# Performance work log

Measured on AMD Instinct MI355X. Metric: run time of the kernel, lower is better.

## Reference

```python
import jax, jax.numpy as jnp
import numpy as np

# Config (matches init_kwargs)
N_HEAD, D_K, D_MODEL, D_INNER, N_LAYERS = 8, 64, 512, 2048, 4
VOCAB, PAD_IDX, REP_IDX, N_POSITION = 512, 0, 1, 200
B, N_NEAR, S = 64, 32, 12  # B batches, 32 near-POIs each, <=12 type tokens per POI
NPOI = B * N_NEAR


def sinusoid_table(n_position, d):
    pos = np.arange(n_position)[:, None].astype(np.float64)
    i = np.arange(d)[None, :]
    angle = pos / np.power(10000.0, 2 * (i // 2) / d)
    tab = np.zeros((n_position, d))
    tab[:, 0::2] = np.sin(angle[:, 0::2])
    tab[:, 1::2] = np.cos(angle[:, 1::2])
    return jnp.asarray(tab, jnp.float32)


def layer_norm(x, g, b, eps=1e-6):
    m = jnp.mean(x, -1, keepdims=True)
    v = jnp.var(x, -1, keepdims=True)
    return g * (x - m) * jax.lax.rsqrt(v + eps) + b


def pack_indices(npl, ttn):
    """Replace the torch Python-loop ragged pack with a single precomputed gather.
    Returns per-output-slot (poi_idx, tok_idx) and a validity mask [B, L]."""
    npl = np.asarray(npl); ttn = np.asarray(ttn)
    Bn = len(npl)
    ends = np.cumsum(npl); starts = ends - npl
    seq_len = np.array([1 + int(ttn[starts[b]:ends[b]].sum()) for b in range(Bn)])
    L = int(seq_len.max())  # == max_batch_len in the torch code
    poi_idx = np.zeros((Bn, L), np.int32)
    tok_idx = np.zeros((Bn, L), np.int32)
    for b in range(Bn):
        pos = 1  # slot 0 is the [REP] token
        for p in range(int(starts[b]), int(ends[b])):
            t = int(ttn[p])
            poi_idx[b, pos:pos + t] = p
            tok_idx[b, pos:pos + t] = np.arange(t)
            pos += t
    valid = np.arange(L)[None, :] < seq_len[:, None]  # pad_from_num_list(pad_num)
    return poi_idx, tok_idx, valid


def setup_inputs() -> dict:
    key = jax.random.key(0)
    ks = jax.random.split(key, 24)
    nrm = lambda k, shape, s=0.02: jax.random.normal(k, shape, jnp.float32) * s
    poi_type = jax.random.randint(ks[0], (NPOI, S), 0, VOCAB, jnp.int32)
    loc_emb = jax.random.normal(ks[1], (NPOI, D_MODEL), jnp.float32)
    near_pois_num_list = jnp.full((B,), N_NEAR, jnp.int32)
    type_token_num = jax.random.randint(ks[2], (NPOI,), 1, S + 1, jnp.int32)
    emb = nrm(ks[3], (VOCAB, D_MODEL), 1.0).at[PAD_IDX].set(0.0)  # padding_idx row zeroed
    return {
        "poi_type": poi_type, "loc_emb": loc_emb,
        "near_pois_num_list": near_pois_num_list, "type_token_num": type_token_num,
        "emb": emb,
        "Wq": nrm(ks[4], (N_LAYERS, D_MODEL, D_MODEL)),
        "Wk": nrm(ks[5], (N_LAYERS, D_MODEL, D_MODEL)),
        "Wv": nrm(ks[6], (N_LAYERS, D_MODEL, D_MODEL)),
        "Wo": nrm(ks[7], (N_LAYERS, D_MODEL, D_MODEL)),
        "bo": jnp.zeros((N_LAYERS, D_MODEL), jnp.float32),
        "ln1_g": jnp.ones((N_LAYERS, D_MODEL), jnp.float32),
        "ln1_b": jnp.zeros((N_LAYERS, D_MODEL), jnp.float32),
        "W1": nrm(ks[8], (N_LAYERS, D_MODEL, D_INNER)),
        "b1": jnp.zeros((N_LAYERS, D_INNER), jnp.float32),
        "W2": nrm(ks[9], (N_LAYERS, D_INNER, D_MODEL)),
        "b2": jnp.zeros((N_LAYERS, D_MODEL), jnp.float32),
        "ln2_g": jnp.ones((N_LAYERS, D_MODEL), jnp.float32),
        "ln2_b": jnp.zeros((N_LAYERS, D_MODEL), jnp.float32),
        "lnf_g": jnp.ones((D_MODEL,), jnp.float32),
        "lnf_b": jnp.zeros((D_MODEL,), jnp.float32),
    }


def encoder_forward(poi_type, loc_emb, poi_idx, tok_idx, tok_mask, attn_mask,
                    emb, Wq, Wk, Wv, Wo, bo, ln1_g, ln1_b, W1, b1, W2, b2,
                    ln2_g, ln2_b, lnf_g, lnf_b):
    pos_table = sinusoid_table(N_POSITION, D_MODEL)
    # embedding + positional encoding (dropout = eval/identity) + location broadcast
    enc = emb[poi_type] + pos_table[None, :S, :] + loc_emb[:, None, :]  # [NPOI, S, D]
    # fused ragged gather+pad (replaces the per-row torch.cat loop)
    x = jnp.where(tok_mask[..., None], enc[poi_idx, tok_idx], 0.0)      # [B, L, D]
    x = x.at[:, 0, :].set(emb[REP_IDX])                                  # [REP] token at slot 0
    x = layer_norm(x, lnf_g, lnf_b)
    Bn, L, D = x.shape
    inv_temp = np.float32(1.0 / np.sqrt(D_K))
    for l in range(N_LAYERS):
        # multi-head self-attention, post-LN residual
        q = (x @ Wq[l]).reshape(Bn, L, N_HEAD, D_K)
        k = (x @ Wk[l]).reshape(Bn, L, N_HEAD, D_K)
        v = (x @ Wv[l]).reshape(Bn, L, N_HEAD, D_K)
        scores = jnp.einsum('bqhd,bkhd->bhqk', q, k) * inv_temp
        scores = jnp.where(attn_mask[:, None, None, :], scores, -1e9)
        attn = jax.nn.softmax(scores, axis=-1)
        o = jnp.einsum('bhqk,bkhd->bqhd', attn, v).reshape(Bn, L, D)
        x = layer_norm(x + o @ Wo[l] + bo[l], ln1_g[l], ln1_b[l])
        # position-wise FFN, post-LN residual
        h = jax.nn.relu(x @ W1[l] + b1[l])
        x = layer_norm(x + h @ W2[l] + b2[l], ln2_g[l], ln2_b[l])
    return x


def reference(poi_type, loc_emb, near_pois_num_list, type_token_num,
              emb, Wq, Wk, Wv, Wo, bo, ln1_g, ln1_b, W1, b1, W2, b2,
              ln2_g, ln2_b, lnf_g, lnf_b):
    poi_idx, tok_idx, valid = pack_indices(np.asarray(near_pois_num_list),
                                           np.asarray(type_token_num))
    L = valid.shape[1]
    tok_mask = jnp.asarray(valid & (np.arange(L)[None, :] > 0))
    attn_mask = jnp.asarray(valid)
    out = encoder_forward(poi_type, loc_emb, jnp.asarray(poi_idx), jnp.asarray(tok_idx),
                          tok_mask, attn_mask, emb, Wq, Wk, Wv, Wo, bo,
                          ln1_g, ln1_b, W1, b1, W2, b2, ln2_g, ln2_b, lnf_g, lnf_b)
    return out, attn_mask
```

## Files before the change

### kernel.cpp

```cpp
#include <hip/hip_runtime.h>
#include <stdint.h>

#define DM 512
#define NH 8
#define DKH 64
#define DI 2048
#define NLAY 4
#define SMAX 12
#define BATCH 64
#define NPOI 2048
#define REPIDX 1
#define VOCAB 512

#define PLS 40
#define PLS2 264

#define S_POI 0
#define S_LOC 1
#define S_NPL 2
#define S_TTN 3
#define S_EMB 4
#define S_WQ 5
#define S_WK 6
#define S_WV 7
#define S_WO 8
#define S_BO 9
#define S_LN1G 10
#define S_LN1B 11
#define S_W1 12
#define S_B1 13
#define S_W2 14
#define S_B2 15
#define S_LN2G 16
#define S_LN2B 17
#define S_LNFG 18
#define S_LNFB 19

#define F_FD 0
#define F_SI 1

typedef unsigned short u16;
typedef short short8 __attribute__((ext_vector_type(8)));
typedef float f32x4 __attribute__((ext_vector_type(4)));
typedef const uint32_t __attribute__((address_space(1)))* as1_u32p;
typedef uint32_t __attribute__((address_space(3)))* as3_u32p;

__device__ __forceinline__ float bf2f(u16 u) {
    union { uint32_t i; float f; } v; v.i = (uint32_t)u << 16; return v.f;
}
__device__ __forceinline__ u16 f2bf(float f) {
    union { uint32_t i; float f; } v; v.f = f;
    uint32_t u = v.i;
    u += 0x7fffu + ((u >> 16) & 1u);
    return (u16)(u >> 16);
}
__device__ __forceinline__ float loadIn(const void* p, size_t i, int fd) {
    if (fd == 1) return bf2f(((const u16*)p)[i]);
    if (fd == 3) { union { u16 u; _Float16 h; } v; v.u = ((const u16*)p)[i]; return (float)v.h; }
    if (fd == 2) return (float)((const double*)p)[i];
    return ((const float*)p)[i];
}
__device__ __forceinline__ int loadInt(const void* p, size_t i, int istride) {
    return (int)((const uint32_t*)p)[i * istride];
}

__device__ __forceinline__ int xcd_swizzle(int lin, int nwg) {
    int qq = nwg >> 3, rr = nwg & 7;
    int xcd = lin & 7, off = lin >> 3;
    return (xcd < rr ? xcd * (qq + 1) : rr * (qq + 1) + (xcd - rr) * qq) + off;
}

__global__ void bind_kernel(void* a0, void* a1, void* a2, void* a3, void* a4,
                            void* c0, void* c1, void* c2, void* c3, void* c4, void* c5, void* c6,
                            void* f0, void* f1,
                            void* w40, void* w41,
                            void* poi, void* npl, void* emb, void* b1,
                            void** tab, int* flags) {
    if (threadIdx.x != 0 || blockIdx.x != 0) return;

    int fd = -1, gAt = -1;
    {
        const u16* a16 = (const u16*)f0; const uint32_t* a32 = (const uint32_t*)f0;
        const unsigned long long* a64 = (const unsigned long long*)f0;
        if (a16[0] == 0x3C00 && a16[1] == 0x3C00) { fd = 3; gAt = 0; }
        else if (a16[0] == 0x3F80 && a16[1] == 0x3F80) { fd = 1; gAt = 0; }
        else if (a32[0] == 0x3F800000u) { fd = 0; gAt = 0; }
        else if (a64[0] == 0x3FF0000000000000ull) { fd = 2; gAt = 0; }
        else {
            const u16* b16 = (const u16*)f1; const uint32_t* b32 = (const uint32_t*)f1;
            const unsigned long long* b64 = (const unsigned long long*)f1;
            if (b16[0] == 0x3C00 && b16[1] == 0x3C00) { fd = 3; gAt = 1; }
            else if (b16[0] == 0x3F80 && b16[1] == 0x3F80) { fd = 1; gAt = 1; }
            else if (b32[0] == 0x3F800000u) { fd = 0; gAt = 1; }
            else if (b64[0] == 0x3FF0000000000000ull) { fd = 2; gAt = 1; }
        }
        if (fd < 0) { fd = 0; gAt = 0; }
    }

    int sI = 1;
    {
        const uint32_t* n32 = (const uint32_t*)npl;
        if (n32[0] == 32u && n32[1] == 0u && n32[2] == 32u) sI = 2;
    }

    void* g1[5] = {a0, a1, a2, a3, a4};
    int locIdx = -1;
    for (int j = 0; j < 5 && locIdx < 0; ++j) {
        float mx = 0.f;
        for (int s = 0; s < 64; ++s) {
            float v = loadIn(g1[j], (size_t)s * 997 + 13, fd);
            mx = fmaxf(mx, fabsf(v));
        }
        if (mx > 0.5f) locIdx = j;
    }
    if (locIdx < 0) locIdx = 0;
    tab[S_LOC] = g1[locIdx];
    {
        int wslot[4] = {S_WQ, S_WK, S_WV, S_WO}; int wi = 0;
        for (int j = 0; j < 5; ++j) if (j != locIdx) tab[wslot[wi++]] = g1[j];
    }

    void* g2[7] = {c0, c1, c2, c3, c4, c5, c6};
    int ttnIdx = -1;
    for (int j = 0; j < 7 && ttnIdx < 0; ++j) {
        const uint32_t* u = (const uint32_t*)g2[j];
        bool ok = true;
        for (int s = 0; s < 24; ++s) {
            uint32_t lo = u[(size_t)s * sI];
            if (lo < 1u || lo > 12u) { ok = false; break; }
            if (sI == 2 && u[(size_t)s * 2 + 1] != 0u) { ok = false; break; }
        }
        if (ok) ttnIdx = j;
    }
    if (ttnIdx < 0) ttnIdx = 0;
    tab[S_TTN] = g2[ttnIdx];
    {
        int gslots[2] = {S_LN1G, S_LN2G}; int bslots[4] = {S_BO, S_LN1B, S_B2, S_LN2B};
        int gi = 0, bi = 0;
        for (int j = 0; j < 7; ++j) {
            if (j == ttnIdx) continue;
            float v0 = loadIn(g2[j], 0, fd);
            if (v0 > 0.5f && gi < 2) tab[gslots[gi++]] = g2[j];
            else if (bi < 4) tab[bslots[bi++]] = g2[j];
            else if (gi < 2) tab[gslots[gi++]] = g2[j];
        }
    }

    tab[S_LNFG] = gAt == 0 ? f0 : f1;
    tab[S_LNFB] = gAt == 0 ? f1 : f0;
    tab[S_W1] = w40; tab[S_W2] = w41;
    tab[S_POI] = poi; tab[S_NPL] = npl; tab[S_EMB] = emb; tab[S_B1] = b1;

    flags[F_FD] = fd;
    flags[F_SI] = sI;
}

__global__ void bind_positional(void* p0, void* p1, void* p2, void* p3, void* p4,
                                void* p5, void* p6, void* p7, void* p8, void* p9,
                                void* p10, void* p11, void* p12, void* p13, void* p14,
                                void* p15, void* p16, void* p17, void* p18, void* p19,
                                void** tab, int* flags) {
    if (threadIdx.x != 0) return;
    void* ps[20] = {p0,p1,p2,p3,p4,p5,p6,p7,p8,p9,p10,p11,p12,p13,p14,p15,p16,p17,p18,p19};
    for (int i = 0; i < 20; ++i) tab[i] = ps[i];
    flags[F_FD] = 0; flags[F_SI] = 1;
}

__global__ void sinusoid_kernel(float* __restrict__ tab) {
    int i = blockIdx.x * 256 + threadIdx.x;
    if (i >= SMAX * DM) return;
    int s = i / DM, d = i - s * DM;
    double expo = (double)(2 * (d / 2)) / (double)DM;
    double angle = (double)s / pow(10000.0, expo);
    tab[i] = (float)((d & 1) ? cos(angle) : sin(angle));
}

__global__ void pack_kernel(void* const* tab, const int* flags,
                            int* __restrict__ seq_len, int* __restrict__ poi_idx,
                            int* __restrict__ tok_idx, int L) {
    const void* npl = tab[S_NPL];
    const void* ttn = tab[S_TTN];
    const int sI = flags[F_SI];
    int b = threadIdx.x;
    if (b >= BATCH) return;
    int start = 0;
    for (int i = 0; i < b; ++i) start += loadInt(npl, i, sI);
    int cnt = loadInt(npl, b, sI);
    for (int j = 0; j < L; ++j) { poi_idx[b * L + j] = 0; tok_idx[b * L + j] = 0; }
    int pos = 1;
    for (int p = start; p < start + cnt; ++p) {
        int tn = loadInt(ttn, p, sI);
        for (int j = 0; j < tn; ++j) {
            if (pos < L) { poi_idx[b * L + pos] = p; tok_idx[b * L + pos] = j; ++pos; }
        }
    }
    seq_len[b] = pos;
}

__global__ __launch_bounds__(256) void build_enc(void* const* tab, const int* flags,
                                                 const float* __restrict__ pos_tab,
                                                 float* __restrict__ enc) {
    const int fd = flags[F_FD], sI = flags[F_SI];
    const void* poi_type = tab[S_POI];
    const void* loc_emb = tab[S_LOC];
    const void* emb = tab[S_EMB];
    int ps = blockIdx.x;
    int p = ps / SMAX, s = ps - p * SMAX;
    int tok = loadInt(poi_type, ps, sI);
    tok = tok < 0 ? 0 : (tok >= VOCAB ? VOCAB - 1 : tok);
    #pragma unroll
    for (int j = 0; j < 2; ++j) {
        int d = threadIdx.x + 256 * j;
        enc[(size_t)ps * DM + d] = loadIn(emb, (size_t)tok * DM + d, fd)
                                 + pos_tab[s * DM + d]
                                 + loadIn(loc_emb, (size_t)p * DM + d, fd);
    }
}

__global__ __launch_bounds__(256) void gather_ln_wave(void* const* tab, const int* flags,
                                                      const float* __restrict__ enc,
                                                      const int* __restrict__ poi_idx,
                                                      const int* __restrict__ tok_idx,
                                                      const int* __restrict__ seq_len,
                                                      float* __restrict__ x, u16* __restrict__ xb,
                                                      int L, int M) {
    const int fd = flags[F_FD];
    const void* emb = tab[S_EMB];
    const void* g = tab[S_LNFG];
    const void* bb = tab[S_LNFB];
    const int row = blockIdx.x * 4 + (threadIdx.x >> 6);
    if (row >= M) return;
    const int b = row / L, l = row - b * L;
    const int lane = threadIdx.x & 63;
    const int slen = seq_len[b];
    float e[8];
    if (l == 0) {
        #pragma unroll
        for (int j = 0; j < 8; ++j) e[j] = loadIn(emb, REPIDX * DM + lane + 64 * j, fd);
    } else if (l < slen) {
        int p = poi_idx[row];
        p = p < 0 ? 0 : (p >= NPOI ? NPOI - 1 : p);
        int t = tok_idx[row];
        t = t < 0 ? 0 : (t >= SMAX ? SMAX - 1 : t);
        const float* src = enc + ((size_t)p * SMAX + t) * DM;
        #pragma unroll
        for (int j = 0; j < 8; ++j) e[j] = src[lane + 64 * j];
    } else {
        #pragma unroll
        for (int j = 0; j < 8; ++j) e[j] = 0.f;
    }
    float s1 = 0.f, s2 = 0.f;
    #pragma unroll
    for (int j = 0; j < 8; ++j) { s1 += e[j]; s2 += e[j] * e[j]; }
    #pragma unroll
    for (int off = 1; off < 64; off <<= 1) {
        s1 += __shfl_xor(s1, off, 64);
        s2 += __shfl_xor(s2, off, 64);
    }
    float mean = s1 * (1.f / DM);
    float var = s2 * (1.f / DM) - mean * mean;
    float rs = rsqrtf(fmaxf(var, 0.f) + 1e-6f);
    #pragma unroll
    for (int j = 0; j < 8; ++j) {
        int d = lane + 64 * j;
        float o = loadIn(g, d, fd) * (e[j] - mean) * rs + loadIn(bb, d, fd);
        x[(size_t)row * DM + d] = o;
        xb[(size_t)row * DM + d] = f2bf(o);
    }
}

__global__ __launch_bounds__(256) void ln_wave(void* const* tab, const int* flags,
                                               float* __restrict__ x, const u16* __restrict__ t,
                                               int gslot, int bslot, int poff,
                                               u16* __restrict__ xb, int M) {
    const int fd = flags[F_FD];
    const void* g = tab[gslot];
    const void* bb = tab[bslot];
    const int row = blockIdx.x * 4 + (threadIdx.x >> 6);
    if (row >= M) return;
    const int lane = threadIdx.x & 63;
    float e[8];
    #pragma unroll
    for (int j = 0; j < 8; ++j) {
        int d = lane + 64 * j;
        e[j] = x[(size_t)row * DM + d] + bf2f(t[(size_t)row * DM + d]);
    }
    float s1 = 0.f, s2 = 0.f;
    #pragma unroll
    for (int j = 0; j < 8; ++j) { s1 += e[j]; s2 += e[j] * e[j]; }
    #pragma unroll
    for (int off = 1; off < 64; off <<= 1) {
        s1 += __shfl_xor(s1, off, 64);
        s2 += __shfl_xor(s2, off, 64);
    }
    float mean = s1 * (1.f / DM);
    float var = s2 * (1.f / DM) - mean * mean;
    float rs = rsqrtf(fmaxf(var, 0.f) + 1e-6f);
    #pragma unroll
    for (int j = 0; j < 8; ++j) {
        int d = lane + 64 * j;
        float o = loadIn(g, poff + d, fd) * (e[j] - mean) * rs + loadIn(bb, poff + d, fd);
        x[(size_t)row * DM + d] = o;
        xb[(size_t)row * DM + d] = f2bf(o);
    }
}

__global__ __launch_bounds__(256) void transpose_tiled(void* const* tab, const int* flags,
                                                       int srcslot, u16* __restrict__ dst,
                                                       int K, int N,
                                                       size_t srcStride, size_t dstStride) {
    __shared__ float ts[32][33];
    const int fd = flags[F_FD];
    const void* src = tab[srcslot];
    const int layer = blockIdx.y;
    const size_t soff = (size_t)layer * srcStride;
    u16* d = dst + (size_t)layer * dstStride;
    const int ntx = N >> 5;
    const int kt = blockIdx.x / ntx, nt = blockIdx.x - kt * ntx;
    const int tx = threadIdx.x & 31, ty = threadIdx.x >> 5;
    #pragma unroll
    for (int j = 0; j < 4; ++j)
        ts[ty + j * 8][tx] = loadIn(src, soff + (size_t)(kt * 32 + ty + j * 8) * N + nt * 32 + tx, fd);
    __syncthreads();
    #pragma unroll
    for (int j = 0; j < 4; ++j)
        d[(size_t)(nt * 32 + ty + j * 8) * K + kt * 32 + tx] = f2bf(ts[tx][ty + j * 8]);
}

__global__ void zero_u16(u16* __restrict__ p, int n) {
    int i = blockIdx.x * 256 + threadIdx.x;
    if (i < n) p[i] = 0;
}
__global__ void zero_vt(u16* __restrict__ vt, int L, int Lr) {
    int tail = Lr - L;
    int n = BATCH * DM * tail;
    int i = blockIdx.x * 256 + threadIdx.x;
    if (i < n) {
        int rd = i / tail;
        int kk = L + (i - rd * tail);
        vt[(size_t)rd * Lr + kk] = 0;
    }
}

template <bool RELU>
__global__ __launch_bounds__(512) void gemm_mfma(const u16* __restrict__ A, const u16* __restrict__ Bt,
                                                 void* const* tab, const int* flags,
                                                 int biasslot, int boff,
                                                 u16* __restrict__ C, int N, int K) {
    __shared__ __align__(16) u16 As[128 * 64];
    __shared__ __align__(16) u16 Bs[128 * 64];
    const int tid = threadIdx.x;
    const int lane = tid & 63;
    const int w = tid >> 6;
    const int wr = w & 3, wc = w >> 2;
    const int gy = gridDim.y;
    int lin = xcd_swizzle(blockIdx.x + gridDim.x * blockIdx.y, gridDim.x * gy);
    const int m0 = (lin / gy) * 128, n0 = (lin % gy) * 128;

    const int sr = tid >> 3;
    const int scb = (((lane & 7) ^ ((lane >> 3) & 7)) * 8);
    const int row_in = lane & 15;
    const int hi4 = lane >> 4;

    f32x4 acc[2][4];
    const f32x4 fz = {0.f, 0.f, 0.f, 0.f};
    #pragma unroll
    for (int i = 0; i < 2; ++i)
        #pragma unroll
        for (int j = 0; j < 4; ++j) acc[i][j] = fz;

    for (int k0 = 0; k0 < K; k0 += 64) {
        __syncthreads();
        #pragma unroll
        for (int j = 0; j < 2; ++j) {
            __builtin_amdgcn_global_load_lds(
                (as1_u32p)(const void*)(A + (size_t)(m0 + j * 64 + sr) * K + k0 + scb),
                (as3_u32p)(void*)(As + j * 4096 + w * 512), 16, 0, 0);
            __builtin_amdgcn_global_load_lds(
                (as1_u32p)(const void*)(Bt + (size_t)(n0 + j * 64 + sr) * K + k0 + scb),
                (as3_u32p)(void*)(Bs + j * 4096 + w * 512), 16, 0, 0);
        }
        __syncthreads();

        #pragma unroll
        for (int kk = 0; kk < 2; ++kk) {
            const int cb = ((kk * 4 + hi4) ^ (row_in & 7)) * 8;
            short8 af[2], bfr[4];
            #pragma unroll
            for (int mf = 0; mf < 2; ++mf)
                af[mf] = *(const short8*)&As[(wr * 32 + mf * 16 + row_in) * 64 + cb];
            #pragma unroll
            for (int nf = 0; nf < 4; ++nf)
                bfr[nf] = *(const short8*)&Bs[(wc * 64 + nf * 16 + row_in) * 64 + cb];
            #pragma unroll
            for (int mf = 0; mf < 2; ++mf)
                #pragma unroll
                for (int nf = 0; nf < 4; ++nf)
                    acc[mf][nf] = __builtin_amdgcn_mfma_f32_16x16x32_bf16(af[mf], bfr[nf], acc[mf][nf], 0, 0, 0);
        }
    }

    const int fd = flags[F_FD];
    #pragma unroll
    for (int nf = 0; nf < 4; ++nf) {
        int col = n0 + wc * 64 + nf * 16 + (lane & 15);
        float bv = (biasslot >= 0) ? loadIn(tab[biasslot], boff + col, fd) : 0.f;
        #pragma unroll
        for (int mf = 0; mf < 2; ++mf) {
            int rbase = m0 + wr * 32 + mf * 16 + (lane >> 4) * 4;
            #pragma unroll
            for (int r = 0; r < 4; ++r) {
                float v = acc[mf][nf][r] + bv;
                if (RELU) v = v > 0.f ? v : 0.f;
                C[(size_t)(rbase + r) * N + col] = f2bf(v);
            }
        }
    }
}

__global__ __launch_bounds__(512) void gemm_qkv(const u16* __restrict__ A, const u16* __restrict__ Bt,
                                                u16* __restrict__ qk, u16* __restrict__ vt,
                                                int L, int Lr, int M, int Mp) {
    __shared__ __align__(16) u16 As[128 * 64];
    __shared__ __align__(16) u16 Bs[128 * 64];
    const int tid = threadIdx.x;
    const int lane = tid & 63;
    const int w = tid >> 6;
    const int wr = w & 3, wc = w >> 2;
    const int gy = gridDim.y;
    int lin = xcd_swizzle(blockIdx.x + gridDim.x * blockIdx.y, gridDim.x * gy);
    const int m0 = (lin / gy) * 128, n0 = (lin % gy) * 128;

    const int sr = tid >> 3;
    const int scb = (((lane & 7) ^ ((lane >> 3) & 7)) * 8);
    const int row_in = lane & 15;
    const int hi4 = lane >> 4;

    f32x4 acc[2][4];
    const f32x4 fz = {0.f, 0.f, 0.f, 0.f};
    #pragma unroll
    for (int i = 0; i < 2; ++i)
        #pragma unroll
        for (int j = 0; j < 4; ++j) acc[i][j] = fz;

    for (int k0 = 0; k0 < DM; k0 += 64) {
        __syncthreads();
        #pragma unroll
        for (int j = 0; j < 2; ++j) {
            __builtin_amdgcn_global_load_lds(
                (as1_u32p)(const void*)(A + (size_t)(m0 + j * 64 + sr) * DM + k0 + scb),
                (as3_u32p)(void*)(As + j * 4096 + w * 512), 16, 0, 0);
            __builtin_amdgcn_global_load_lds(
                (as1_u32p)(const void*)(Bt + (size_t)(n0 + j * 64 + sr) * DM + k0 + scb),
                (as3_u32p)(void*)(Bs + j * 4096 + w * 512), 16, 0, 0);
        }
        __syncthreads();

        #pragma unroll
        for (int kk = 0; kk < 2; ++kk) {
            const int cb = ((kk * 4 + hi4) ^ (row_in & 7)) * 8;
            short8 af[2], bfr[4];
            #pragma unroll
            for (int mf = 0; mf < 2; ++mf)
                af[mf] = *(const short8*)&As[(wr * 32 + mf * 16 + row_in) * 64 + cb];
            #pragma unroll
            for (int nf = 0; nf < 4; ++nf)
                bfr[nf] = *(const short8*)&Bs[(wc * 64 + nf * 16 + row_in) * 64 + cb];
            #pragma unroll
            for (int mf = 0; mf < 2; ++mf)
                #pragma unroll
                for (int nf = 0; nf < 4; ++nf)
                    acc[mf][nf] = __builtin_amdgcn_mfma_f32_16x16x32_bf16(af[mf], bfr[nf], acc[mf][nf], 0, 0, 0);
        }
    }

    const size_t MpDM = (size_t)Mp * DM;
    #pragma unroll
    for (int mf = 0; mf < 2; ++mf) {
        #pragma unroll
        for (int r = 0; r < 4; ++r) {
            int row = m0 + wr * 32 + mf * 16 + (lane >> 4) * 4 + r;
            int bb2 = row / L;
            int ltok = row - bb2 * L;
            #pragma unroll
            for (int nf = 0; nf < 4; ++nf) {
                int col = n0 + wc * 64 + nf * 16 + (lane & 15);
                float v = acc[mf][nf][r];
                if (col < 1024) {
                    qk[(size_t)(col >> 9) * MpDM + (size_t)row * DM + (col & 511)] = f2bf(v);
                } else if (row < M) {
                    vt[((size_t)bb2 * DM + (col - 1024)) * Lr + ltok] = f2bf(v);
                }
            }
        }
    }
}

__global__ __launch_bounds__(256) void attn_flash16(const u16* __restrict__ q, const u16* __restrict__ k,
                                                    const u16* __restrict__ vt, u16* __restrict__ o,
                                                    const int* __restrict__ seq_len,
                                                    int L, int Lr, int M, int nq4) {
    __shared__ __align__(16) u16 pl[4][16 * PLS2];
    const int tid = threadIdx.x;
    const int lane = tid & 63;
    const int w = tid >> 6;
    const int wgid = xcd_swizzle(blockIdx.x, gridDim.x);
    const int b = wgid / (nq4 * NH);
    const int rem = wgid - b * nq4 * NH;
    const int h = rem / nq4;
    const int q4 = rem - h * nq4;
    const int nk = (L + 15) >> 4;
    int qt = q4 * 4 + w;
    if (qt >= nk) qt = nk - 1;
    const int slen = seq_len[b];
    const size_t base = (size_t)b * L;
    const int hcol = h * DKH;
    const int col = lane & 15;
    const int hi = lane >> 4;
    const int k8 = hi * 8;
    u16* plw = &pl[w][0];

    size_t qrr = base + qt * 16 + col;
    if (qrr >= (size_t)M) qrr = (size_t)M - 1;
    const short8 qf0 = *(const short8*)&q[qrr * DM + hcol + k8];
    const short8 qf1 = *(const short8*)&q[qrr * DM + hcol + 32 + k8];

    const u16* vbase = vt + ((size_t)b * DM + hcol) * Lr;

    f32x4 sc[16];
    const f32x4 fz = {0.f, 0.f, 0.f, 0.f};
    #pragma unroll
    for (int kt = 0; kt < 16; ++kt) sc[kt] = fz;
    #pragma unroll
    for (int kt = 0; kt < 16; ++kt) {
        if (kt < nk) {
            size_t krr = base + kt * 16 + col;
            if (krr >= (size_t)M) krr = (size_t)M - 1;
            short8 kf0 = *(const short8*)&k[krr * DM + hcol + k8];
            short8 kf1 = *(const short8*)&k[krr * DM + hcol + 32 + k8];
            f32x4 a = fz;
            a = __builtin_amdgcn_mfma_f32_16x16x32_bf16(qf0, kf0, a, 0, 0, 0);
            a = __builtin_amdgcn_mfma_f32_16x16x32_bf16(qf1, kf1, a, 0, 0, 0);
            sc[kt] = a;
        }
    }

    float mx[4] = {-1e30f, -1e30f, -1e30f, -1e30f};
    #pragma unroll
    for (int kt = 0; kt < 16; ++kt) {
        const bool kv = (kt < nk) && ((kt * 16 + col) < slen);
        #pragma unroll
        for (int r = 0; r < 4; ++r) {
            float s = kv ? sc[kt][r] * 0.125f : -1e30f;
            sc[kt][r] = s;
            mx[r] = fmaxf(mx[r], s);
        }
    }
    #pragma unroll
    for (int r = 0; r < 4; ++r) {
        #pragma unroll
        for (int off = 1; off < 16; off <<= 1)
            mx[r] = fmaxf(mx[r], __shfl_xor(mx[r], off, 64));
    }
    float sum[4] = {0.f, 0.f, 0.f, 0.f};
    #pragma unroll
    for (int kt = 0; kt < 16; ++kt) {
        #pragma unroll
        for (int r = 0; r < 4; ++r) {
            float p = __expf(sc[kt][r] - mx[r]);
            sum[r] += p;
            plw[(hi * 4 + r) * PLS2 + kt * 16 + col] = f2bf(p);
        }
    }
    #pragma unroll
    for (int r = 0; r < 4; ++r) {
        #pragma unroll
        for (int off = 1; off < 16; off <<= 1)
            sum[r] += __shfl_xor(sum[r], off, 64);
    }

    f32x4 oacc[4];
    #pragma unroll
    for (int dt = 0; dt < 4; ++dt) oacc[dt] = fz;
    const int nchunk = (nk + 1) >> 1;
    for (int c = 0; c < nchunk; ++c) {
        short8 pa = *(const short8*)&plw[col * PLS2 + c * 32 + k8];
        #pragma unroll
        for (int dt = 0; dt < 4; ++dt) {
            short8 vf = *(const short8*)&vbase[(size_t)(dt * 16 + col) * Lr + c * 32 + k8];
            oacc[dt] = __builtin_amdgcn_mfma_f32_16x16x32_bf16(pa, vf, oacc[dt], 0, 0, 0);
        }
    }

    #pragma unroll
    for (int r = 0; r < 4; ++r) {
        int qr = qt * 16 + hi * 4 + r;
        if (qr < L) {
            float inv = 1.f / sum[r];
            #pragma unroll
            for (int dt = 0; dt < 4; ++dt)
                o[(base + qr) * DM + hcol + dt * 16 + col] = f2bf(oacc[dt][r] * inv);
        }
    }
}

__global__ __launch_bounds__(256) void attn_flash(const u16* __restrict__ q, const u16* __restrict__ k,
                                                  const u16* __restrict__ vt, u16* __restrict__ o,
                                                  const int* __restrict__ seq_len,
                                                  int L, int Lr, int M, int nq4) {
    __shared__ __align__(16) u16 pl[4][16 * PLS];
    const int tid = threadIdx.x;
    const int lane = tid & 63;
    const int w = tid >> 6;
    const int wgid = xcd_swizzle(blockIdx.x, gridDim.x);
    const int b = wgid / (nq4 * NH);
    const int rem = wgid - b * nq4 * NH;
    const int h = rem / nq4;
    const int q4 = rem - h * nq4;
    const int nk = (L + 15) >> 4;
    int qt = q4 * 4 + w;
    if (qt >= nk) qt = nk - 1;
    const int slen = seq_len[b];
    const size_t base = (size_t)b * L;
    const int hcol = h * DKH;
    const int col = lane & 15;
    const int hi = lane >> 4;
    const int k8 = hi * 8;
    u16* plw = &pl[w][0];

    size_t qrr = base + qt * 16 + col;
    if (qrr >= (size_t)M) qrr = (size_t)M - 1;
    const short8 qf0 = *(const short8*)&q[qrr * DM + hcol + k8];
    const short8 qf1 = *(const short8*)&q[qrr * DM + hcol + 32 + k8];

    const u16* vbase = vt + ((size_t)b * DM + hcol) * Lr;

    f32x4 oacc[4];
    #pragma unroll
    for (int dt = 0; dt < 4; ++dt) oacc[dt] = (f32x4){0.f, 0.f, 0.f, 0.f};
    float m[4] = {-1e30f, -1e30f, -1e30f, -1e30f};
    float ll[4] = {0.f, 0.f, 0.f, 0.f};

    const int nchunk = (nk + 1) >> 1;
    for (int c = 0; c < nchunk; ++c) {
        const int kt0 = c * 2, kt1 = c * 2 + 1;
        f32x4 s0, s1;
        {
            size_t krr = base + kt0 * 16 + col;
            if (krr >= (size_t)M) krr = (size_t)M - 1;
            short8 kf0 = *(const short8*)&k[krr * DM + hcol + k8];
            short8 kf1 = *(const short8*)&k[krr * DM + hcol + 32 + k8];
            f32x4 a = {0.f, 0.f, 0.f, 0.f};
            a = __builtin_amdgcn_mfma_f32_16x16x32_bf16(qf0, kf0, a, 0, 0, 0);
            a = __builtin_amdgcn_mfma_f32_16x16x32_bf16(qf1, kf1, a, 0, 0, 0);
            s0 = a;
        }
        {
            size_t krr = base + kt1 * 16 + col;
            if (krr >= (size_t)M) krr = (size_t)M - 1;
            short8 kf0 = *(const short8*)&k[krr * DM + hcol + k8];
            short8 kf1 = *(const short8*)&k[krr * DM + hcol + 32 + k8];
            f32x4 a = {0.f, 0.f, 0.f, 0.f};
            a = __builtin_amdgcn_mfma_f32_16x16x32_bf16(qf0, kf0, a, 0, 0, 0);
            a = __builtin_amdgcn_mfma_f32_16x16x32_bf16(qf1, kf1, a, 0, 0, 0);
            s1 = a;
        }
        const bool v0 = (kt0 * 16 + col) < slen;
        const bool v1 = (kt1 < nk) && ((kt1 * 16 + col) < slen);
        float cm[4];
        #pragma unroll
        for (int r = 0; r < 4; ++r) {
            float a0 = v0 ? s0[r] * 0.125f : -1e30f;
            float a1 = v1 ? s1[r] * 0.125f : -1e30f;
            s0[r] = a0; s1[r] = a1;
            cm[r] = fmaxf(a0, a1);
        }
        #pragma unroll
        for (int r = 0; r < 4; ++r) {
            #pragma unroll
            for (int off = 1; off < 16; off <<= 1)
                cm[r] = fmaxf(cm[r], __shfl_xor(cm[r], off, 64));
        }
        float scr[4];
        #pragma unroll
        for (int r = 0; r < 4; ++r) {
            float nm = fmaxf(m[r], cm[r]);
            scr[r] = __expf(m[r] - nm);
            m[r] = nm;
        }
        #pragma unroll
        for (int dt = 0; dt < 4; ++dt)
            #pragma unroll
            for (int r = 0; r < 4; ++r) oacc[dt][r] *= scr[r];
        #pragma unroll
        for (int r = 0; r < 4; ++r) {
            float p0 = __expf(s0[r] - m[r]);
            float p1 = __expf(s1[r] - m[r]);
            ll[r] = ll[r] * scr[r] + p0 + p1;
            plw[(hi * 4 + r) * PLS + col] = f2bf(p0);
            plw[(hi * 4 + r) * PLS + 16 + col] = f2bf(p1);
        }
        short8 pa = *(const short8*)&plw[col * PLS + k8];
        #pragma unroll
        for (int dt = 0; dt < 4; ++dt) {
            short8 vf = *(const short8*)&vbase[(size_t)(dt * 16 + col) * Lr + c * 32 + k8];
            oacc[dt] = __builtin_amdgcn_mfma_f32_16x16x32_bf16(pa, vf, oacc[dt], 0, 0, 0);
        }
    }

    #pragma unroll
    for (int r = 0; r < 4; ++r) {
        #pragma unroll
        for (int off = 1; off < 16; off <<= 1)
            ll[r] += __shfl_xor(ll[r], off, 64);
    }
    #pragma unroll
    for (int r = 0; r < 4; ++r) {
        int qr = qt * 16 + hi * 4 + r;
        if (qr < L) {
            float inv = 1.f / ll[r];
            #pragma unroll
            for (int dt = 0; dt < 4; ++dt)
                o[(base + qr) * DM + hcol + dt * 16 + col] = f2bf(oacc[dt][r] * inv);
        }
    }
}

__global__ void store_out(const float* __restrict__ x, float* __restrict__ out, int n) {
    int i = blockIdx.x * 256 + threadIdx.x;
    if (i < n) out[i] = x[i];
}
__global__ void store_mask(const int* __restrict__ seq_len, float* __restrict__ out, int L, int M) {
    int i = blockIdx.x * 256 + threadIdx.x;
    if (i < M) {
        int b = i / L, l = i - b * L;
        out[i] = (l < seq_len[b]) ? 1.0f : 0.0f;
    }
}

extern "C" void kernel_launch(void* const* d_in, const int* in_sizes, int n_in,
                              void* d_out, int out_size, void* d_ws, size_t ws_size,
                              hipStream_t stream) {
    const int L = out_size / (BATCH * (DM + 1));
    const int M = BATCH * L;
    const int Mp = (M + 127) & ~127;
    const int Lr = (L + 31) & ~31;
    const int nk = (L + 15) >> 4;
    const int nq4 = (nk + 3) >> 2;

    uint8_t* p = (uint8_t*)d_ws;
    auto carve = [&](size_t bytes) -> void* {
        void* r = (void*)p;
        p += (bytes + 255) & ~(size_t)255;
        return r;
    };
    void** tab = (void**)carve(20 * sizeof(void*));
    int* flags = (int*)carve(8 * 4);
    int* seq_len = (int*)carve((size_t)BATCH * 4);
    int* poi_idx = (int*)carve((size_t)M * 4);
    int* tok_idx = (int*)carve((size_t)M * 4);
    float* pos_tab = (float*)carve((size_t)SMAX * DM * 4);
    float* x = (float*)carve((size_t)Mp * DM * 4);
    u16* t = (u16*)carve((size_t)Mp * DM * 2);
    u16* xb = (u16*)carve((size_t)Mp * DM * 2);
    const size_t MpDM = (size_t)Mp * DM;
    const size_t vt_bytes = (size_t)BATCH * DM * Lr * 2;
    size_t region_bytes = (size_t)Mp * DI * 2;
    size_t qkv_bytes = 3 * MpDM * 2 + vt_bytes;
    size_t enc_bytes = (size_t)NPOI * SMAX * DM * 4;
    if (qkv_bytes > region_bytes) region_bytes = qkv_bytes;
    if (enc_bytes > region_bytes) region_bytes = enc_bytes;
    u16* region = (u16*)carve(region_bytes);
    const size_t SQ = (size_t)DM * DM;
    const size_t SF = (size_t)DM * DI;
    const size_t PST = 4 * SQ + 2 * SF;
    u16* WT4 = (u16*)carve(PST * NLAY * 2);

    float* enc = (float*)region;
    u16* qb = region;
    u16* kb = region + MpDM;
    u16* ob = region + 2 * MpDM;
    u16* vt = region + 3 * MpDM;

    int g1M[8], n1M = 0, g2k[8], n2k = 0, g4M[4], n4M = 0, g512[4], n512 = 0;
    int idx_poi = -1, idx_npl = -1, idx_emb = -1, idx_b1 = -1;
    int cpoi = 0, cnpl = 0, cemb = 0, cb1 = 0;
    for (int i = 0; i < n_in; ++i) {
        switch (in_sizes[i]) {
            case 24576: idx_poi = i; ++cpoi; break;
            case 64: idx_npl = i; ++cnpl; break;
            case 262144: idx_emb = i; ++cemb; break;
            case 8192: idx_b1 = i; ++cb1; break;
            case 1048576: if (n1M < 8) g1M[n1M] = i; ++n1M; break;
            case 2048: if (n2k < 8) g2k[n2k] = i; ++n2k; break;
            case 4194304: if (n4M < 4) g4M[n4M] = i; ++n4M; break;
            case 512: if (n512 < 4) g512[n512] = i; ++n512; break;
            default: break;
        }
    }
    bool census = (n_in == 20) && cpoi == 1 && cnpl == 1 && cemb == 1 && cb1 == 1 &&
                  n1M == 5 && n2k == 7 && n4M == 2 && n512 == 2;

    if (census) {
        bind_kernel<<<1, 1, 0, stream>>>(
            d_in[g1M[0]], d_in[g1M[1]], d_in[g1M[2]], d_in[g1M[3]], d_in[g1M[4]],
            d_in[g2k[0]], d_in[g2k[1]], d_in[g2k[2]], d_in[g2k[3]], d_in[g2k[4]], d_in[g2k[5]], d_in[g2k[6]],
            d_in[g512[0]], d_in[g512[1]],
            d_in[g4M[0]], d_in[g4M[1]],
            d_in[idx_poi], d_in[idx_npl], d_in[idx_emb], d_in[idx_b1],
            tab, flags);
    } else {
        void* q[20];
        for (int i = 0; i < 20; ++i) q[i] = (i < n_in) ? d_in[i] : d_in[0];
        bind_positional<<<1, 1, 0, stream>>>(q[0], q[1], q[2], q[3], q[4], q[5], q[6], q[7], q[8], q[9],
                                             q[10], q[11], q[12], q[13], q[14], q[15], q[16], q[17], q[18], q[19],
                                             tab, flags);
    }

    sinusoid_kernel<<<(SMAX * DM + 255) / 256, 256, 0, stream>>>(pos_tab);
    pack_kernel<<<1, 64, 0, stream>>>(tab, flags, seq_len, poi_idx, tok_idx, L);
    build_enc<<<NPOI * SMAX, 256, 0, stream>>>(tab, flags, pos_tab, enc);
    gather_ln_wave<<<dim3((M + 3) / 4), 256, 0, stream>>>(tab, flags, enc, poi_idx, tok_idx, seq_len, x, xb, L, M);
    if (Mp > M) {
        int nz = (Mp - M) * DM;
        zero_u16<<<(nz + 255) / 256, 256, 0, stream>>>(xb + (size_t)M * DM, nz);
    }

    {
        dim3 gTQ(16 * 16, NLAY);
        transpose_tiled<<<gTQ, 256, 0, stream>>>(tab, flags, S_WQ, WT4,            DM, DM, SQ, PST);
        transpose_tiled<<<gTQ, 256, 0, stream>>>(tab, flags, S_WK, WT4 + SQ,       DM, DM, SQ, PST);
        transpose_tiled<<<gTQ, 256, 0, stream>>>(tab, flags, S_WV, WT4 + 2 * SQ,   DM, DM, SQ, PST);
        transpose_tiled<<<gTQ, 256, 0, stream>>>(tab, flags, S_WO, WT4 + 3 * SQ,   DM, DM, SQ, PST);
        dim3 gT1(16 * 64, NLAY);
        transpose_tiled<<<gT1, 256, 0, stream>>>(tab, flags, S_W1, WT4 + 4 * SQ,   DM, DI, SF, PST);
        dim3 gT2(64 * 16, NLAY);
        transpose_tiled<<<gT2, 256, 0, stream>>>(tab, flags, S_W2, WT4 + 4 * SQ + SF, DI, DM, SF, PST);
    }

    if (Lr > L) {
        const int vtTail = (Lr - L) * BATCH * DM;
        zero_vt<<<(vtTail + 255) / 256, 256, 0, stream>>>(vt, L, Lr);
    }

    dim3 gP(Mp / 128, DM / 128);
    dim3 gQKV(Mp / 128, 1536 / 128);
    dim3 gF(Mp / 128, DI / 128);
    dim3 gLN((M + 3) / 4);
    dim3 gAF(nq4 * NH * BATCH);
    for (int l = 0; l < NLAY; ++l) {
        u16* WL = WT4 + (size_t)l * PST;
        gemm_qkv<<<gQKV, 512, 0, stream>>>(xb, WL, region, vt, L, Lr, M, Mp);
        if (nk <= 16)
            attn_flash16<<<gAF, 256, 0, stream>>>(qb, kb, vt, ob, seq_len, L, Lr, M, nq4);
        else
            attn_flash<<<gAF, 256, 0, stream>>>(qb, kb, vt, ob, seq_len, L, Lr, M, nq4);
        gemm_mfma<false><<<gP, 512, 0, stream>>>(ob, WL + 3 * SQ, tab, flags, S_BO, l * DM, t, DM, DM);
        ln_wave<<<gLN, 256, 0, stream>>>(tab, flags, x, t, S_LN1G, S_LN1B, l * DM, xb, M);
        gemm_mfma<true><<<gF, 512, 0, stream>>>(xb, WL + 4 * SQ, tab, flags, S_B1, l * DI, region, DI, DM);
        gemm_mfma<false><<<gP, 512, 0, stream>>>(region, WL + 4 * SQ + SF, tab, flags, S_B2, l * DM, t, DM, DI);
        ln_wave<<<gLN, 256, 0, stream>>>(tab, flags, x, t, S_LN2G, S_LN2B, l * DM, xb, M);
    }

    float* out = (float*)d_out;
    store_out<<<(M * DM + 255) / 256, 256, 0, stream>>>(x, out, M * DM);
    store_mask<<<(M + 255) / 256, 256, 0, stream>>>(seq_len, out + (size_t)M * DM, L, M);
}
```

Measured before the change: 1.339 ms.

## Double-buffer LDS tiles in GEMM kernels to overlap loads with MFMA

Both the generic MFMA GEMM and the fused QKV GEMM now keep two LDS buffers per operand. The next K-tile is issued with global_load_lds into the spare buffer while MFMAs consume the current one, leaving one barrier per iteration instead of two. The goal is to hide global-memory latency behind matrix compute. In exchange, shared memory per block doubles to 64 KB, which may limit how many blocks fit on a CU.

```diff
diff --git a/kernel.cpp b/kernel.cpp
--- a/kernel.cpp
+++ b/kernel.cpp
@@ -347,8 +347,8 @@
                                                  void* const* tab, const int* flags,
                                                  int biasslot, int boff,
                                                  u16* __restrict__ C, int N, int K) {
-    __shared__ __align__(16) u16 As[128 * 64];
-    __shared__ __align__(16) u16 Bs[128 * 64];
+    __shared__ __align__(16) u16 As[2][128 * 64];
+    __shared__ __align__(16) u16 Bs[2][128 * 64];
     const int tid = threadIdx.x;
     const int lane = tid & 63;
     const int w = tid >> 6;
@@ -362,42 +362,49 @@
     const int row_in = lane & 15;
     const int hi4 = lane >> 4;
 
-    f32x4 acc[2][4];
-    const f32x4 fz = {0.f, 0.f, 0.f, 0.f};
-    #pragma unroll
-    for (int i = 0; i < 2; ++i)
-        #pragma unroll
-        for (int j = 0; j < 4; ++j) acc[i][j] = fz;
-
-    for (int k0 = 0; k0 < K; k0 += 64) {
-        __syncthreads();
+    auto STAGE = [&](int buf, int k0) {
         #pragma unroll
         for (int j = 0; j < 2; ++j) {
             __builtin_amdgcn_global_load_lds(
                 (as1_u32p)(const void*)(A + (size_t)(m0 + j * 64 + sr) * K + k0 + scb),
-                (as3_u32p)(void*)(As + j * 4096 + w * 512), 16, 0, 0);
+                (as3_u32p)(void*)(As[buf] + j * 4096 + w * 512), 16, 0, 0);
             __builtin_amdgcn_global_load_lds(
                 (as1_u32p)(const void*)(Bt + (size_t)(n0 + j * 64 + sr) * K + k0 + scb),
-                (as3_u32p)(void*)(Bs + j * 4096 + w * 512), 16, 0, 0);
-        }
-        __syncthreads();
-
+                (as3_u32p)(void*)(Bs[buf] + j * 4096 + w * 512), 16, 0, 0);
+        }
+    };
+
+    f32x4 acc[2][4];
+    const f32x4 fz = {0.f, 0.f, 0.f, 0.f};
+    #pragma unroll
+    for (int i = 0; i < 2; ++i)
+        #pragma unroll
+        for (int j = 0; j < 4; ++j) acc[i][j] = fz;
+
+    const int nt = K >> 6;
+    STAGE(0, 0);
+    __syncthreads();
+    int cur = 0;
+    for (int t = 0; t < nt; ++t) {
+        if (t + 1 < nt) STAGE(cur ^ 1, (t + 1) * 64);
         #pragma unroll
         for (int kk = 0; kk < 2; ++kk) {
             const int cb = ((kk * 4 + hi4) ^ (row_in & 7)) * 8;
             short8 af[2], bfr[4];
             #pragma unroll
             for (int mf = 0; mf < 2; ++mf)
-                af[mf] = *(const short8*)&As[(wr * 32 + mf * 16 + row_in) * 64 + cb];
+                af[mf] = *(const short8*)&As[cur][(wr * 32 + mf * 16 + row_in) * 64 + cb];
             #pragma unroll
             for (int nf = 0; nf < 4; ++nf)
-                bfr[nf] = *(const short8*)&Bs[(wc * 64 + nf * 16 + row_in) * 64 + cb];
+                bfr[nf] = *(const short8*)&Bs[cur][(wc * 64 + nf * 16 + row_in) * 64 + cb];
             #pragma unroll
             for (int mf = 0; mf < 2; ++mf)
                 #pragma unroll
                 for (int nf = 0; nf < 4; ++nf)
                     acc[mf][nf] = __builtin_amdgcn_mfma_f32_16x16x32_bf16(af[mf], bfr[nf], acc[mf][nf], 0, 0, 0);
         }
+        __syncthreads();
+        cur ^= 1;
     }
 
     const int fd = flags[F_FD];
@@ -421,8 +428,8 @@
 __global__ __launch_bounds__(512) void gemm_qkv(const u16* __restrict__ A, const u16* __restrict__ Bt,
                                                 u16* __restrict__ qk, u16* __restrict__ vt,
                                                 int L, int Lr, int M, int Mp) {
-    __shared__ __align__(16) u16 As[128 * 64];
-    __shared__ __align__(16) u16 Bs[128 * 64];
+    __shared__ __align__(16) u16 As[2][128 * 64];
+    __shared__ __align__(16) u16 Bs[2][128 * 64];
     const int tid = threadIdx.x;
     const int lane = tid & 63;
     const int w = tid >> 6;
@@ -436,42 +443,49 @@
     const int row_in = lane & 15;
     const int hi4 = lane >> 4;
 
-    f32x4 acc[2][4];
-    const f32x4 fz = {0.f, 0.f, 0.f, 0.f};
-    #pragma unroll
-    for (int i = 0; i < 2; ++i)
-        #pragma unroll
-        for (int j = 0; j < 4; ++j) acc[i][j] = fz;
-
-    for (int k0 = 0; k0 < DM; k0 += 64) {
-        __syncthreads();
+    auto STAGE = [&](int buf, int k0) {
         #pragma unroll
         for (int j = 0; j < 2; ++j) {
             __builtin_amdgcn_global_load_lds(
                 (as1_u32p)(const void*)(A + (size_t)(m0 + j * 64 + sr) * DM + k0 + scb),
-                (as3_u32p)(void*)(As + j * 4096 + w * 512), 16, 0, 0);
+                (as3_u32p)(void*)(As[buf] + j * 4096 + w * 512), 16, 0, 0);
             __builtin_amdgcn_global_load_lds(
                 (as1_u32p)(const void*)(Bt + (size_t)(n0 + j * 64 + sr) * DM + k0 + scb),
-                (as3_u32p)(void*)(Bs + j * 4096 + w * 512), 16, 0, 0);
-        }
-        __syncthreads();
-
+                (as3_u32p)(void*)(Bs[buf] + j * 4096 + w * 512), 16, 0, 0);
+        }
+    };
+
+    f32x4 acc[2][4];
+    const f32x4 fz = {0.f, 0.f, 0.f, 0.f};
+    #pragma unroll
+    for (int i = 0; i < 2; ++i)
+        #pragma unroll
+        for (int j = 0; j < 4; ++j) acc[i][j] = fz;
+
+    const int nt = DM >> 6;
+    STAGE(0, 0);
+    __syncthreads();
+    int cur = 0;
+    for (int t = 0; t < nt; ++t) {
+        if (t + 1 < nt) STAGE(cur ^ 1, (t + 1) * 64);
         #pragma unroll
         for (int kk = 0; kk < 2; ++kk) {
             const int cb = ((kk * 4 + hi4) ^ (row_in & 7)) * 8;
             short8 af[2], bfr[4];
             #pragma unroll
             for (int mf = 0; mf < 2; ++mf)
-                af[mf] = *(const short8*)&As[(wr * 32 + mf * 16 + row_in) * 64 + cb];
+                af[mf] = *(const short8*)&As[cur][(wr * 32 + mf * 16 + row_in) * 64 + cb];
             #pragma unroll
             for (int nf = 0; nf < 4; ++nf)
-                bfr[nf] = *(const short8*)&Bs[(wc * 64 + nf * 16 + row_in) * 64 + cb];
+                bfr[nf] = *(const short8*)&Bs[cur][(wc * 64 + nf * 16 + row_in) * 64 + cb];
             #pragma unroll
             for (int mf = 0; mf < 2; ++mf)
                 #pragma unroll
                 for (int nf = 0; nf < 4; ++nf)
                     acc[mf][nf] = __builtin_amdgcn_mfma_f32_16x16x32_bf16(af[mf], bfr[nf], acc[mf][nf], 0, 0, 0);
         }
+        __syncthreads();
+        cur ^= 1;
     }
 
     const size_t MpDM = (size_t)Mp * DM;
```

Result: faster. 1.307 ms (-2.4%).
